# Kernel optimization log

Measured on AMD Instinct MI355X. Metric: run time of the kernel, lower is better.

Reference implementation:

```python
import jax, jax.numpy as jnp
import numpy as np

B, S, D, H = 2, 2048, 1024, 16
DH = D // H  # head_dim = 64


def setup_inputs() -> dict:
    key = jax.random.key(0)
    ks = jax.random.split(key, 10)
    inp = {
        "query": jax.random.normal(ks[0], (B, S, D), jnp.float32),
        "key": jax.random.normal(ks[1], (B, S, D), jnp.float32),
        "value": jax.random.normal(ks[2], (B, S, D), jnp.float32),
        "mask": jnp.ones((B, S), jnp.int32),
        # per-head q/k/v projections stacked over the head axis [H, D, DH]
        "Wq": jax.random.normal(ks[3], (H, D, DH), jnp.float32) * 0.02,
        "bq": jnp.zeros((H, DH), jnp.float32),
        "Wk": jax.random.normal(ks[4], (H, D, DH), jnp.float32) * 0.02,
        "bk": jnp.zeros((H, DH), jnp.float32),
        "Wv": jax.random.normal(ks[5], (H, D, DH), jnp.float32) * 0.02,
        "bv": jnp.zeros((H, DH), jnp.float32),
        # output projection fc: Linear(D, D)
        "Wo": jax.random.normal(ks[6], (D, D), jnp.float32) * 0.02,
        "bo": jnp.zeros((D,), jnp.float32),
    }
    return inp


def reference(query, key, value, mask, Wq, bq, Wk, bk, Wv, bv, Wo, bo):
    scale = 1.0 / jnp.sqrt(jnp.asarray(DH, query.dtype))
    # batched per-head projections: [B,S,D] x [H,D,DH] -> [B,H,S,DH]
    q = jnp.einsum('bsd,hde->bhse', query, Wq) + bq[None, :, None, :]
    k = jnp.einsum('bsd,hde->bhse', key, Wk) + bk[None, :, None, :]
    v = jnp.einsum('bsd,hde->bhse', value, Wv) + bv[None, :, None, :]
    # scaled dot-product attention scores [B,H,Sq,Sk]
    scores = jnp.einsum('bhqe,bhke->bhqk', q, k) * scale
    scores = jnp.where(mask[:, None, None, :] == 0, jnp.asarray(-1e9, scores.dtype), scores)
    attn = jax.nn.softmax(scores, axis=-1)
    ctx = jnp.einsum('bhqk,bhke->bhqe', attn, v)          # [B,H,S,DH]
    ctx = ctx.transpose(0, 2, 1, 3).reshape(query.shape[0], -1, H * DH)  # concat heads
    return ctx @ Wo + bo
```

## Files before the change

kernel.cpp:

```cpp
#include <hip/hip_runtime.h>
#include <stdint.h>
#include <math.h>


typedef __attribute__((ext_vector_type(8))) short short8;
typedef __attribute__((ext_vector_type(4))) short short4b;
typedef __attribute__((ext_vector_type(4))) float floatx4;

#define LOG2E 1.44269504088896340736f

__device__ __forceinline__ unsigned short f32_bf16(float f) {
  union { float f; unsigned u; } c; c.f = f;
  return (unsigned short)((c.u + 0x7FFFu + ((c.u >> 16) & 1u)) >> 16);
}
__device__ __forceinline__ float bf16_f32(unsigned short u) {
  union { unsigned u; float f; } c; c.u = ((unsigned)u) << 16;
  return c.f;
}
__device__ __forceinline__ void gld16(const void* g, void* l) {
  __builtin_amdgcn_global_load_lds((const __attribute__((address_space(1))) void*)g,
                                   (__attribute__((address_space(3))) void*)l, 16, 0, 0);
}
__device__ __forceinline__ short4b pack_bf16x4(float a0, float a1, float a2, float a3) {
  union { float f; unsigned u; } c0, c1, c2, c3;
  c0.f = a0; c1.f = a1; c2.f = a2; c3.f = a3;
  union { unsigned u[2]; short4b s; } r;
  r.u[0] = __builtin_amdgcn_perm(c1.u, c0.u, 0x07060302u);
  r.u[1] = __builtin_amdgcn_perm(c3.u, c2.u, 0x07060302u);
  return r.s;
}


__global__ __launch_bounds__(256) void cvt3_kernel(
    const float* __restrict__ a, const float* __restrict__ b, const float* __restrict__ c,
    unsigned short* __restrict__ oa, unsigned short* __restrict__ ob, unsigned short* __restrict__ oc,
    const int* __restrict__ mask, float* __restrict__ mb, int n4) {
  int i = blockIdx.x * 256 + threadIdx.x;
  if (blockIdx.y == 0 && blockIdx.x < 16) {
    int j = blockIdx.x * 256 + threadIdx.x;
    mb[j] = (mask[j] == 0) ? (-1.0e9f * LOG2E) : 0.0f;
  }
  if (i >= n4) return;
  const float* in; unsigned short* out;
  if (blockIdx.y == 0) { in = a; out = oa; }
  else if (blockIdx.y == 1) { in = b; out = ob; }
  else { in = c; out = oc; }
  float4 v = reinterpret_cast<const float4*>(in)[i];
  ushort4 o;
  o.x = f32_bf16(v.x); o.y = f32_bf16(v.y); o.z = f32_bf16(v.z); o.w = f32_bf16(v.w);
  reinterpret_cast<ushort4*>(out)[i] = o;
}

__global__ __launch_bounds__(256) void transpose_w_kernel(
    const float* __restrict__ w0, const float* __restrict__ w1, const float* __restrict__ w2,
    const float* __restrict__ wo,
    unsigned short* __restrict__ o0, unsigned short* __restrict__ o1, unsigned short* __restrict__ o2,
    unsigned short* __restrict__ oo) {
  __shared__ float t[32][33];
  const int tx = threadIdx.x & 31, ty = threadIdx.x >> 5;
  const int zb = blockIdx.z;
  const float* in; unsigned short* out; int R, C, z, r0, c0;
  if (zb < 48) {
    if (blockIdx.y >= 2) return;
    const int sel = zb >> 4; z = zb & 15;
    in = (sel == 0) ? w0 : (sel == 1) ? w1 : w2;
    out = (sel == 0) ? o0 : (sel == 1) ? o1 : o2;
    R = 1024; C = 64;
  } else {
    in = wo; out = oo; R = 1024; C = 1024; z = 0;
  }
  r0 = blockIdx.x * 32; c0 = blockIdx.y * 32;
  const float* inp = in + (size_t)z * R * C;
  #pragma unroll
  for (int j = 0; j < 4; ++j)
    t[ty + j * 8][tx] = inp[(size_t)(r0 + ty + j * 8) * C + c0 + tx];
  __syncthreads();
  #pragma unroll
  for (int j = 0; j < 4; ++j)
    out[((size_t)z * C + c0 + ty + j * 8) * R + r0 + tx] = f32_bf16(t[tx][ty + j * 8]);
}

__global__ __launch_bounds__(256) void transpose_v_kernel(
    const unsigned short* __restrict__ in, unsigned short* __restrict__ out, int R, int C) {
  __shared__ unsigned short t[32][33];
  const int z = blockIdx.z;
  const unsigned short* inp = in + (size_t)z * R * C;
  const int r0 = blockIdx.x * 32, c0 = blockIdx.y * 32;
  const int tx = threadIdx.x & 31, ty = threadIdx.x >> 5;
  #pragma unroll
  for (int j = 0; j < 4; ++j)
    t[ty + j * 8][tx] = inp[(size_t)(r0 + ty + j * 8) * C + c0 + tx];
  __syncthreads();
  #pragma unroll
  for (int j = 0; j < 4; ++j)
    out[((size_t)z * C + c0 + ty + j * 8) * R + r0 + tx] = t[tx][ty + j * 8];
}


__device__ __forceinline__ void gemm_core(
    const unsigned short* __restrict__ A, const unsigned short* __restrict__ Bt,
    int K, int blockM, int blockN,
    unsigned short* As, unsigned short* Bs, floatx4 acc[4][4]) {
  const int tid = threadIdx.x;
  const int w = tid >> 6;
  const int lane = tid & 63;
  const int quad = lane >> 4, l15 = lane & 15;
  const int wm = w & 1, wn = w >> 1;
  const int srow = lane >> 2;
  const int scol = (lane & 3) * 8;

  #pragma unroll
  for (int mi = 0; mi < 4; ++mi)
    #pragma unroll
    for (int ni = 0; ni < 4; ++ni)
      acc[mi][ni] = (floatx4){0.f, 0.f, 0.f, 0.f};

  const unsigned short* Arow = A + (size_t)blockM * K;
  const unsigned short* Brow = Bt + (size_t)blockN * K;

  for (int k0 = 0; k0 < K; k0 += 32) {
    #pragma unroll
    for (int i = 0; i < 2; ++i) {
      int row = w * 32 + i * 16;
      gld16(Arow + (size_t)(row + srow) * K + k0 + scol, As + row * 32);
      gld16(Brow + (size_t)(row + srow) * K + k0 + scol, Bs + row * 32);
    }
    __syncthreads();
    short8 bf[4];
    #pragma unroll
    for (int ni = 0; ni < 4; ++ni)
      bf[ni] = *(const short8*)(Bs + (wn * 64 + ni * 16 + l15) * 32 + quad * 8);
    #pragma unroll
    for (int mi = 0; mi < 4; ++mi) {
      short8 af = *(const short8*)(As + (wm * 64 + mi * 16 + l15) * 32 + quad * 8);
      #pragma unroll
      for (int ni = 0; ni < 4; ++ni)
        acc[mi][ni] = __builtin_amdgcn_mfma_f32_16x16x32_bf16(af, bf[ni], acc[mi][ni], 0, 0, 0);
    }
    __syncthreads();
  }
}

struct ProjArgs {
  const unsigned short* A[3];
  const unsigned short* Bt[3];
  const float* bias[3];
  unsigned short* out[3];
};

__global__ __launch_bounds__(256) void gemm_proj_kernel(ProjArgs pa, int K) {
  __shared__ unsigned short As[128 * 32];
  __shared__ unsigned short Bs[128 * 32];
  const int z = blockIdx.z;
  const int blockN = blockIdx.x * 128, blockM = blockIdx.y * 128;
  floatx4 acc[4][4];
  gemm_core(pa.A[z], pa.Bt[z], K, blockM, blockN, As, Bs, acc);

  const float* bias = pa.bias[z];
  unsigned short* outp = pa.out[z];
  const int tid = threadIdx.x, w = tid >> 6, lane = tid & 63;
  const int quad = lane >> 4, l15 = lane & 15;
  const int wm = w & 1, wn = w >> 1;
  #pragma unroll
  for (int mi = 0; mi < 4; ++mi)
    #pragma unroll
    for (int ni = 0; ni < 4; ++ni) {
      const int n = blockN + wn * 64 + ni * 16 + l15;
      const int h = n >> 6, e = n & 63;
      const float bv = bias[n];
      #pragma unroll
      for (int r = 0; r < 4; ++r) {
        const int m = blockM + wm * 64 + mi * 16 + quad * 4 + r;
        const int b = m >> 11, s = m & 2047;
        outp[(((size_t)b * 16 + h) * 2048 + s) * 64 + e] = f32_bf16(acc[mi][ni][r] + bv);
      }
    }
}

__global__ __launch_bounds__(256) void gemm_out_kernel(
    const unsigned short* __restrict__ A, const unsigned short* __restrict__ Bt,
    const float* __restrict__ bias, float* __restrict__ out, int K, int N) {
  __shared__ unsigned short As[128 * 32];
  __shared__ unsigned short Bs[64 * 32];
  const int tid = threadIdx.x;
  const int w = tid >> 6, lane = tid & 63;
  const int quad = lane >> 4, l15 = lane & 15;
  const int wm = w & 1, wn = w >> 1;
  const int srow = lane >> 2;
  const int scol = (lane & 3) * 8;
  const int blockN = blockIdx.x * 64, blockM = blockIdx.y * 128;

  floatx4 acc[4][2];
  #pragma unroll
  for (int mi = 0; mi < 4; ++mi)
    #pragma unroll
    for (int ni = 0; ni < 2; ++ni)
      acc[mi][ni] = (floatx4){0.f, 0.f, 0.f, 0.f};

  const unsigned short* Arow = A + (size_t)blockM * K;
  const unsigned short* Brow = Bt + (size_t)blockN * K;

  for (int k0 = 0; k0 < K; k0 += 32) {
    #pragma unroll
    for (int i = 0; i < 2; ++i) {
      int row = w * 32 + i * 16;
      gld16(Arow + (size_t)(row + srow) * K + k0 + scol, As + row * 32);
    }
    gld16(Brow + (size_t)(w * 16 + srow) * K + k0 + scol, Bs + (w * 16) * 32);
    __syncthreads();
    short8 bf[2];
    #pragma unroll
    for (int ni = 0; ni < 2; ++ni)
      bf[ni] = *(const short8*)(Bs + (wn * 32 + ni * 16 + l15) * 32 + quad * 8);
    #pragma unroll
    for (int mi = 0; mi < 4; ++mi) {
      short8 af = *(const short8*)(As + (wm * 64 + mi * 16 + l15) * 32 + quad * 8);
      #pragma unroll
      for (int ni = 0; ni < 2; ++ni)
        acc[mi][ni] = __builtin_amdgcn_mfma_f32_16x16x32_bf16(af, bf[ni], acc[mi][ni], 0, 0, 0);
    }
    __syncthreads();
  }

  #pragma unroll
  for (int mi = 0; mi < 4; ++mi)
    #pragma unroll
    for (int ni = 0; ni < 2; ++ni) {
      const int n = blockN + wn * 32 + ni * 16 + l15;
      const float bv = bias[n];
      #pragma unroll
      for (int r = 0; r < 4; ++r) {
        const int m = blockM + wm * 64 + mi * 16 + quad * 4 + r;
        out[(size_t)m * N + n] = acc[mi][ni][r] + bv;
      }
    }
}


__global__ __launch_bounds__(256) void attn_kernel(
    const unsigned short* __restrict__ Q, const unsigned short* __restrict__ Kg,
    const unsigned short* __restrict__ Vt, const float* __restrict__ maskAdd,
    unsigned short* __restrict__ ctx) {
  const int S = 2048;
  const int tid = threadIdx.x;
  const int w = tid >> 6, lane = tid & 63, quad = lane >> 4, l15 = lane & 15;
  const int qb = blockIdx.x, bh = blockIdx.y;
  const int b = bh >> 4, h = bh & 15;
  const int q0 = qb * 128;

  __shared__ unsigned short Ks[128 * 64];
  __shared__ unsigned short Vs[64 * 128];

  const unsigned short* Qb = Q + (size_t)bh * S * 64;
  const unsigned short* Kb = Kg + (size_t)bh * S * 64;
  const unsigned short* Vb = Vt + (size_t)bh * 64 * S;
  const float* mb = maskAdd + (size_t)b * S;

  const float qs = 0.125f * LOG2E;
  short8 qf[2][2];
  #pragma unroll
  for (int mi = 0; mi < 2; ++mi)
    #pragma unroll
    for (int kq = 0; kq < 2; ++kq) {
      short8 v = *(const short8*)(Qb + (size_t)(q0 + w * 32 + mi * 16 + l15) * 64 + kq * 32 + quad * 8);
      #pragma unroll
      for (int j = 0; j < 8; ++j)
        v[j] = (short)f32_bf16(bf16_f32((unsigned short)v[j]) * qs);
      qf[mi][kq] = v;
    }

  short4b ones4;
  #pragma unroll
  for (int j = 0; j < 4; ++j) ones4[j] = (short)0x3F80;

  floatx4 O[2][4], ls[2];
  #pragma unroll
  for (int mi = 0; mi < 2; ++mi) {
    #pragma unroll
    for (int ne = 0; ne < 4; ++ne) O[mi][ne] = (floatx4){0.f, 0.f, 0.f, 0.f};
    ls[mi] = (floatx4){0.f, 0.f, 0.f, 0.f};
  }

  for (int t = 0; t < 16; ++t) {
    const int kv0 = t * 128;
    __syncthreads();
    #pragma unroll
    for (int i = 0; i < 4; ++i) {
      int r0 = w * 32 + i * 8;
      int row = r0 + (lane >> 3);
      int cg = (lane & 7) ^ (row & 7);
      gld16(Kb + (size_t)(kv0 + row) * 64 + cg * 8, Ks + r0 * 64);
    }
    #pragma unroll
    for (int i = 0; i < 4; ++i) {
      int r0 = w * 16 + i * 4;
      int row = r0 + (lane >> 4);
      int p = lane & 15;
      int cg = (p & 8) | ((p & 7) ^ (row & 7));
      gld16(Vb + (size_t)row * S + kv0 + cg * 8, Vs + r0 * 128);
    }
    __syncthreads();

    #pragma unroll
    for (int ph = 0; ph < 2; ++ph) {
      floatx4 sc[2][4];
      #pragma unroll
      for (int ni = 0; ni < 4; ++ni) {
        const int kt = ph * 4 + ni;
        const int krow = kt * 16 + l15;
        short8 kf0 = *(const short8*)(Ks + krow * 64 + ((quad) ^ (l15 & 7)) * 8);
        short8 kf1 = *(const short8*)(Ks + krow * 64 + ((4 + quad) ^ (l15 & 7)) * 8);
        #pragma unroll
        for (int mi = 0; mi < 2; ++mi) {
          floatx4 s = (floatx4){0.f, 0.f, 0.f, 0.f};
          s = __builtin_amdgcn_mfma_f32_16x16x32_bf16(kf0, qf[mi][0], s, 0, 0, 0);
          s = __builtin_amdgcn_mfma_f32_16x16x32_bf16(kf1, qf[mi][1], s, 0, 0, 0);
          sc[mi][ni] = s;
        }
      }
      #pragma unroll
      for (int ni = 0; ni < 4; ++ni) {
        const int kt = ph * 4 + ni;
        const float4 mav = *(const float4*)(mb + kv0 + kt * 16 + quad * 4);
        short4b pf[2];
        #pragma unroll
        for (int mi = 0; mi < 2; ++mi) {
          float p0 = __builtin_amdgcn_exp2f(sc[mi][ni][0] + mav.x);
          float p1 = __builtin_amdgcn_exp2f(sc[mi][ni][1] + mav.y);
          float p2 = __builtin_amdgcn_exp2f(sc[mi][ni][2] + mav.z);
          float p3 = __builtin_amdgcn_exp2f(sc[mi][ni][3] + mav.w);
          pf[mi] = pack_bf16x4(p0, p1, p2, p3);
        }
        const int c = kt * 2 + (quad >> 1);
        const int pc = (c & 8) | ((c & 7) ^ (l15 & 7));
        #pragma unroll
        for (int ne = 0; ne < 4; ++ne) {
          short4b vf = *(const short4b*)(Vs + (ne * 16 + l15) * 128 + pc * 8 + (quad & 1) * 4);
          #pragma unroll
          for (int mi = 0; mi < 2; ++mi)
            O[mi][ne] = __builtin_amdgcn_mfma_f32_16x16x16bf16_1k(pf[mi], vf, O[mi][ne], 0, 0, 0);
        }
        #pragma unroll
        for (int mi = 0; mi < 2; ++mi)
          ls[mi] = __builtin_amdgcn_mfma_f32_16x16x16bf16_1k(pf[mi], ones4, ls[mi], 0, 0, 0);
      }
    }
  }

  #pragma unroll
  for (int mi = 0; mi < 2; ++mi)
    #pragma unroll
    for (int r = 0; r < 4; ++r) {
      const float inv = __builtin_amdgcn_rcpf(ls[mi][r]);
      const int s = q0 + w * 32 + mi * 16 + quad * 4 + r;
      #pragma unroll
      for (int ne = 0; ne < 4; ++ne)
        ctx[((size_t)b * S + s) * 1024 + h * 64 + ne * 16 + l15] = f32_bf16(O[mi][ne][r] * inv);
    }
}


extern "C" void kernel_launch(void* const* d_in, const int* in_sizes, int n_in,
                              void* d_out, int out_size, void* d_ws, size_t ws_size,
                              hipStream_t stream) {
  const float* query = (const float*)d_in[0];
  const float* key   = (const float*)d_in[1];
  const float* value = (const float*)d_in[2];
  const int*   mask  = (const int*)d_in[3];
  const float* Wq = (const float*)d_in[4];
  const float* bq = (const float*)d_in[5];
  const float* Wk = (const float*)d_in[6];
  const float* bk = (const float*)d_in[7];
  const float* Wv = (const float*)d_in[8];
  const float* bv = (const float*)d_in[9];
  const float* Wo = (const float*)d_in[10];
  const float* bo = (const float*)d_in[11];
  float* out = (float*)d_out;

  char* ws = (char*)d_ws;
  const size_t MB = 1024 * 1024;
  unsigned short* qin  = (unsigned short*)(ws + 0);
  unsigned short* kin  = (unsigned short*)(ws + 8 * MB);
  unsigned short* vin  = (unsigned short*)(ws + 16 * MB);
  unsigned short* WqT  = (unsigned short*)(ws + 24 * MB);
  unsigned short* WkT  = (unsigned short*)(ws + 26 * MB);
  unsigned short* WvT  = (unsigned short*)(ws + 28 * MB);
  unsigned short* WoT  = (unsigned short*)(ws + 30 * MB);
  unsigned short* Qp   = (unsigned short*)(ws + 32 * MB);
  unsigned short* Kp   = (unsigned short*)(ws + 40 * MB);
  unsigned short* Vp   = (unsigned short*)(ws + 48 * MB);
  float* maskAdd       = (float*)(ws + 56 * MB);
  unsigned short* ctxb = qin;
  unsigned short* Vtb  = kin;

  cvt3_kernel<<<dim3(4096, 3), 256, 0, stream>>>(query, key, value, qin, kin, vin,
                                                 mask, maskAdd, 1048576);
  transpose_w_kernel<<<dim3(32, 32, 49), 256, 0, stream>>>(Wq, Wk, Wv, Wo, WqT, WkT, WvT, WoT);

  ProjArgs pa;
  pa.A[0] = qin; pa.A[1] = kin; pa.A[2] = vin;
  pa.Bt[0] = WqT; pa.Bt[1] = WkT; pa.Bt[2] = WvT;
  pa.bias[0] = bq; pa.bias[1] = bk; pa.bias[2] = bv;
  pa.out[0] = Qp; pa.out[1] = Kp; pa.out[2] = Vp;
  gemm_proj_kernel<<<dim3(8, 32, 3), 256, 0, stream>>>(pa, 1024);

  transpose_v_kernel<<<dim3(64, 2, 32), 256, 0, stream>>>(Vp, Vtb, 2048, 64);
  attn_kernel<<<dim3(16, 32), 256, 0, stream>>>(Qp, Kp, Vtb, maskAdd, ctxb);
  gemm_out_kernel<<<dim3(16, 32), 256, 0, stream>>>(ctxb, WoT, bo, out, 1024, 1024);
}
```

Baseline: 272.2 us.

## Fuse V transpose into projection GEMM and stage P through LDS for K=32 MFMA

After: 257.7 us. 5.3% less time.

```diff
diff --git a/kernel.cpp b/kernel.cpp
--- a/kernel.cpp
+++ b/kernel.cpp
@@ -4,7 +4,6 @@
 
 
 typedef __attribute__((ext_vector_type(8))) short short8;
-typedef __attribute__((ext_vector_type(4))) short short4b;
 typedef __attribute__((ext_vector_type(4))) float floatx4;
 
 #define LOG2E 1.44269504088896340736f
@@ -20,14 +19,6 @@
 __device__ __forceinline__ void gld16(const void* g, void* l) {
   __builtin_amdgcn_global_load_lds((const __attribute__((address_space(1))) void*)g,
                                    (__attribute__((address_space(3))) void*)l, 16, 0, 0);
-}
-__device__ __forceinline__ short4b pack_bf16x4(float a0, float a1, float a2, float a3) {
-  union { float f; unsigned u; } c0, c1, c2, c3;
-  c0.f = a0; c1.f = a1; c2.f = a2; c3.f = a3;
-  union { unsigned u[2]; short4b s; } r;
-  r.u[0] = __builtin_amdgcn_perm(c1.u, c0.u, 0x07060302u);
-  r.u[1] = __builtin_amdgcn_perm(c3.u, c2.u, 0x07060302u);
-  return r.s;
 }
 
 
@@ -80,22 +71,6 @@
     out[((size_t)z * C + c0 + ty + j * 8) * R + r0 + tx] = f32_bf16(t[tx][ty + j * 8]);
 }
 
-__global__ __launch_bounds__(256) void transpose_v_kernel(
-    const unsigned short* __restrict__ in, unsigned short* __restrict__ out, int R, int C) {
-  __shared__ unsigned short t[32][33];
-  const int z = blockIdx.z;
-  const unsigned short* inp = in + (size_t)z * R * C;
-  const int r0 = blockIdx.x * 32, c0 = blockIdx.y * 32;
-  const int tx = threadIdx.x & 31, ty = threadIdx.x >> 5;
-  #pragma unroll
-  for (int j = 0; j < 4; ++j)
-    t[ty + j * 8][tx] = inp[(size_t)(r0 + ty + j * 8) * C + c0 + tx];
-  __syncthreads();
-  #pragma unroll
-  for (int j = 0; j < 4; ++j)
-    out[((size_t)z * C + c0 + ty + j * 8) * R + r0 + tx] = t[tx][ty + j * 8];
-}
-
 
 __device__ __forceinline__ void gemm_core(
     const unsigned short* __restrict__ A, const unsigned short* __restrict__ Bt,
@@ -141,40 +116,70 @@
   }
 }
 
-struct ProjArgs {
-  const unsigned short* A[3];
-  const unsigned short* Bt[3];
-  const float* bias[3];
-  unsigned short* out[3];
-};
-
-__global__ __launch_bounds__(256) void gemm_proj_kernel(ProjArgs pa, int K) {
+__global__ __launch_bounds__(256) void gemm_proj_kernel(
+    const unsigned short* __restrict__ qin, const unsigned short* __restrict__ kin,
+    const unsigned short* __restrict__ vin,
+    const unsigned short* __restrict__ WqT, const unsigned short* __restrict__ WkT,
+    const unsigned short* __restrict__ WvT,
+    const float* __restrict__ bq, const float* __restrict__ bk, const float* __restrict__ bv,
+    unsigned short* __restrict__ Qp, unsigned short* __restrict__ Kp,
+    unsigned short* __restrict__ Vt) {
   __shared__ unsigned short As[128 * 32];
   __shared__ unsigned short Bs[128 * 32];
-  const int z = blockIdx.z;
-  const int blockN = blockIdx.x * 128, blockM = blockIdx.y * 128;
+  const int z = blockIdx.y, bx = blockIdx.x;
+  const unsigned short *A, *Bt;
+  const float* bias;
+  int blockM, blockN;
+  if (z < 2) {
+    blockN = (bx & 7) * 128; blockM = (bx >> 3) * 128;
+    A = z ? kin : qin; Bt = z ? WkT : WqT; bias = z ? bk : bq;
+  } else {
+    blockM = (bx & 7) * 128; blockN = (bx >> 3) * 128;
+    A = WvT; Bt = vin; bias = bv;
+  }
   floatx4 acc[4][4];
-  gemm_core(pa.A[z], pa.Bt[z], K, blockM, blockN, As, Bs, acc);
-
-  const float* bias = pa.bias[z];
-  unsigned short* outp = pa.out[z];
+  gemm_core(A, Bt, 1024, blockM, blockN, As, Bs, acc);
+
   const int tid = threadIdx.x, w = tid >> 6, lane = tid & 63;
   const int quad = lane >> 4, l15 = lane & 15;
   const int wm = w & 1, wn = w >> 1;
-  #pragma unroll
-  for (int mi = 0; mi < 4; ++mi)
-    #pragma unroll
-    for (int ni = 0; ni < 4; ++ni) {
-      const int n = blockN + wn * 64 + ni * 16 + l15;
-      const int h = n >> 6, e = n & 63;
-      const float bv = bias[n];
-      #pragma unroll
-      for (int r = 0; r < 4; ++r) {
-        const int m = blockM + wm * 64 + mi * 16 + quad * 4 + r;
-        const int b = m >> 11, s = m & 2047;
-        outp[(((size_t)b * 16 + h) * 2048 + s) * 64 + e] = f32_bf16(acc[mi][ni][r] + bv);
+
+  if (z < 2) {
+    unsigned short* outp = z ? Kp : Qp;
+    #pragma unroll
+    for (int mi = 0; mi < 4; ++mi)
+      #pragma unroll
+      for (int ni = 0; ni < 4; ++ni) {
+        const int n = blockN + wn * 64 + ni * 16 + l15;
+        const int h = n >> 6, e = n & 63;
+        const float bvv = bias[n];
+        #pragma unroll
+        for (int r = 0; r < 4; ++r) {
+          const int m = blockM + wm * 64 + mi * 16 + quad * 4 + r;
+          const int b = m >> 11, s = m & 2047;
+          outp[(((size_t)b * 16 + h) * 2048 + s) * 64 + e] = f32_bf16(acc[mi][ni][r] + bvv);
+        }
       }
-    }
+  } else {
+    #pragma unroll
+    for (int mi = 0; mi < 4; ++mi) {
+      float br[4];
+      #pragma unroll
+      for (int r = 0; r < 4; ++r)
+        br[r] = bias[blockM + wm * 64 + mi * 16 + quad * 4 + r];
+      #pragma unroll
+      for (int ni = 0; ni < 4; ++ni) {
+        const int n = blockN + wn * 64 + ni * 16 + l15;
+        const int b = n >> 11, s = n & 2047;
+        #pragma unroll
+        for (int r = 0; r < 4; ++r) {
+          const int m = blockM + wm * 64 + mi * 16 + quad * 4 + r;
+          const int h = m >> 6, e = m & 63;
+          Vt[(((size_t)b * 16 + h) * 64 + e) * 2048 + s] = f32_bf16(acc[mi][ni][r] + br[r]);
+        }
+      }
+    }
+  }
 }
 
 __global__ __launch_bounds__(256) void gemm_out_kernel(
@@ -237,7 +242,7 @@
 }
 
 
-__global__ __launch_bounds__(256) void attn_kernel(
+__global__ __launch_bounds__(256, 3) void attn_kernel(
     const unsigned short* __restrict__ Q, const unsigned short* __restrict__ Kg,
     const unsigned short* __restrict__ Vt, const float* __restrict__ maskAdd,
     unsigned short* __restrict__ ctx) {
@@ -250,6 +255,8 @@
 
   __shared__ unsigned short Ks[128 * 64];
   __shared__ unsigned short Vs[64 * 128];
+  __shared__ unsigned short Ps[4][32 * 64];
+  unsigned short* Pw = Ps[w];
 
   const unsigned short* Qb = Q + (size_t)bh * S * 64;
   const unsigned short* Kb = Kg + (size_t)bh * S * 64;
@@ -269,9 +276,9 @@
       qf[mi][kq] = v;
     }
 
-  short4b ones4;
-  #pragma unroll
-  for (int j = 0; j < 4; ++j) ones4[j] = (short)0x3F80;
+  short8 onesf;
+  #pragma unroll
+  for (int j = 0; j < 8; ++j) onesf[j] = (short)0x3F80;
 
   floatx4 O[2][4], ls[2];
   #pragma unroll
@@ -299,6 +306,9 @@
       int cg = (p & 8) | ((p & 7) ^ (row & 7));
       gld16(Vb + (size_t)row * S + kv0 + cg * 8, Vs + r0 * 128);
     }
+    float ma[8];
+    #pragma unroll
+    for (int ni = 0; ni < 8; ++ni) ma[ni] = mb[kv0 + ni * 16 + l15];
     __syncthreads();
 
     #pragma unroll
@@ -306,43 +316,52 @@
       floatx4 sc[2][4];
       #pragma unroll
       for (int ni = 0; ni < 4; ++ni) {
-        const int kt = ph * 4 + ni;
-        const int krow = kt * 16 + l15;
-        short8 kf0 = *(const short8*)(Ks + krow * 64 + ((quad) ^ (l15 & 7)) * 8);
-        short8 kf1 = *(const short8*)(Ks + krow * 64 + ((4 + quad) ^ (l15 & 7)) * 8);
+        const int key = (ph * 4 + ni) * 16 + l15;
+        short8 kf0 = *(const short8*)(Ks + key * 64 + ((quad) ^ (l15 & 7)) * 8);
+        short8 kf1 = *(const short8*)(Ks + key * 64 + ((4 + quad) ^ (l15 & 7)) * 8);
         #pragma unroll
         for (int mi = 0; mi < 2; ++mi) {
           floatx4 s = (floatx4){0.f, 0.f, 0.f, 0.f};
-          s = __builtin_amdgcn_mfma_f32_16x16x32_bf16(kf0, qf[mi][0], s, 0, 0, 0);
-          s = __builtin_amdgcn_mfma_f32_16x16x32_bf16(kf1, qf[mi][1], s, 0, 0, 0);
+          s = __builtin_amdgcn_mfma_f32_16x16x32_bf16(qf[mi][0], kf0, s, 0, 0, 0);
+          s = __builtin_amdgcn_mfma_f32_16x16x32_bf16(qf[mi][1], kf1, s, 0, 0, 0);
           sc[mi][ni] = s;
         }
       }
       #pragma unroll
-      for (int ni = 0; ni < 4; ++ni) {
-        const int kt = ph * 4 + ni;
-        const float4 mav = *(const float4*)(mb + kv0 + kt * 16 + quad * 4);
-        short4b pf[2];
+      for (int mi = 0; mi < 2; ++mi)
+        #pragma unroll
+        for (int r = 0; r < 4; ++r) {
+          const int row = mi * 16 + quad * 4 + r;
+          const int g = (row + (row >> 3)) & 7;
+          #pragma unroll
+          for (int ni = 0; ni < 4; ++ni) {
+            float p = __builtin_amdgcn_exp2f(sc[mi][ni][r] + ma[ph * 4 + ni]);
+            union { float f; unsigned u; } c; c.f = p;
+            const int ch = (ni * 2 + (l15 >> 3)) ^ g;
+            Pw[row * 64 + (ch & 7) * 8 + (l15 & 7)] = (unsigned short)(c.u >> 16);
+          }
+        }
+      #pragma unroll
+      for (int kkl = 0; kkl < 2; ++kkl) {
+        const int kk = ph * 2 + kkl;
+        short8 pfr[2], vf[4];
         #pragma unroll
         for (int mi = 0; mi < 2; ++mi) {
-          float p0 = __builtin_amdgcn_exp2f(sc[mi][ni][0] + mav.x);
-          float p1 = __builtin_amdgcn_exp2f(sc[mi][ni][1] + mav.y);
-          float p2 = __builtin_amdgcn_exp2f(sc[mi][ni][2] + mav.z);
-          float p3 = __builtin_amdgcn_exp2f(sc[mi][ni][3] + mav.w);
-          pf[mi] = pack_bf16x4(p0, p1, p2, p3);
-        }
-        const int c = kt * 2 + (quad >> 1);
-        const int pc = (c & 8) | ((c & 7) ^ (l15 & 7));
+          const int gp = (2 * mi + l15 + (l15 >> 3)) & 7;
+          pfr[mi] = *(const short8*)(Pw + (mi * 16 + l15) * 64 + ((kkl * 4 + quad) ^ gp) * 8);
+        }
         #pragma unroll
         for (int ne = 0; ne < 4; ++ne) {
-          short4b vf = *(const short4b*)(Vs + (ne * 16 + l15) * 128 + pc * 8 + (quad & 1) * 4);
+          const int c = kk * 4 + quad;
+          vf[ne] = *(const short8*)(Vs + (ne * 16 + l15) * 128 + ((c & 8) | ((c & 7) ^ (l15 & 7))) * 8);
+        }
+        #pragma unroll
+        for (int mi = 0; mi < 2; ++mi) {
           #pragma unroll
-          for (int mi = 0; mi < 2; ++mi)
-            O[mi][ne] = __builtin_amdgcn_mfma_f32_16x16x16bf16_1k(pf[mi], vf, O[mi][ne], 0, 0, 0);
-        }
-        #pragma unroll
-        for (int mi = 0; mi < 2; ++mi)
-          ls[mi] = __builtin_amdgcn_mfma_f32_16x16x16bf16_1k(pf[mi], ones4, ls[mi], 0, 0, 0);
+          for (int ne = 0; ne < 4; ++ne)
+            O[mi][ne] = __builtin_amdgcn_mfma_f32_16x16x32_bf16(pfr[mi], vf[ne], O[mi][ne], 0, 0, 0);
+          ls[mi] = __builtin_amdgcn_mfma_f32_16x16x32_bf16(pfr[mi], onesf, ls[mi], 0, 0, 0);
+        }
       }
     }
   }
@@ -388,23 +407,15 @@
   unsigned short* WoT  = (unsigned short*)(ws + 30 * MB);
   unsigned short* Qp   = (unsigned short*)(ws + 32 * MB);
   unsigned short* Kp   = (unsigned short*)(ws + 40 * MB);
-  unsigned short* Vp   = (unsigned short*)(ws + 48 * MB);
+  unsigned short* Vt   = (unsigned short*)(ws + 48 * MB);
   float* maskAdd       = (float*)(ws + 56 * MB);
   unsigned short* ctxb = qin;
-  unsigned short* Vtb  = kin;
 
   cvt3_kernel<<<dim3(4096, 3), 256, 0, stream>>>(query, key, value, qin, kin, vin,
                                                  mask, maskAdd, 1048576);
   transpose_w_kernel<<<dim3(32, 32, 49), 256, 0, stream>>>(Wq, Wk, Wv, Wo, WqT, WkT, WvT, WoT);
-
-  ProjArgs pa;
-  pa.A[0] = qin; pa.A[1] = kin; pa.A[2] = vin;
-  pa.Bt[0] = WqT; pa.Bt[1] = WkT; pa.Bt[2] = WvT;
-  pa.bias[0] = bq; pa.bias[1] = bk; pa.bias[2] = bv;
-  pa.out[0] = Qp; pa.out[1] = Kp; pa.out[2] = Vp;
-  gemm_proj_kernel<<<dim3(8, 32, 3), 256, 0, stream>>>(pa, 1024);
-
-  transpose_v_kernel<<<dim3(64, 2, 32), 256, 0, stream>>>(Vp, Vtb, 2048, 64);
-  attn_kernel<<<dim3(16, 32), 256, 0, stream>>>(Qp, Kp, Vtb, maskAdd, ctxb);
+  gemm_proj_kernel<<<dim3(256, 3), 256, 0, stream>>>(qin, kin, vin, WqT, WkT, WvT,
+                                                     bq, bk, bv, Qp, Kp, Vt);
+  attn_kernel<<<dim3(16, 32), 256, 0, stream>>>(Qp, Kp, Vt, maskAdd, ctxb);
   gemm_out_kernel<<<dim3(16, 32), 256, 0, stream>>>(ctxb, WoT, bo, out, 1024, 1024);
 }
```
